# Performance work log

Measured on AMD Instinct MI355X. Metric: run time of the kernel, lower is better.

The kernel has to match this reference:

```python
import jax, jax.numpy as jnp
import numpy as np

B = 16          # number of point clouds in the batch
N_COARSE = 1024 # coarse points per cloud
N_FINE = 4096   # fine (skip) points per cloud
C_IN = 256
C_SKIP = 128
K = 3
EPS = 1e-16


def setup_inputs() -> dict:
    key = jax.random.key(0)
    ks = jax.random.split(key, 8)
    x = jax.random.normal(ks[0], (B * N_COARSE, C_IN), dtype=jnp.float32)
    pos = jax.random.uniform(ks[1], (B * N_COARSE, 3), dtype=jnp.float32)
    x_skip = jax.random.normal(ks[2], (B * N_FINE, C_SKIP), dtype=jnp.float32)
    pos_skip = jax.random.uniform(ks[3], (B * N_FINE, 3), dtype=jnp.float32)
    batch = jnp.repeat(jnp.arange(B, dtype=jnp.int64), N_COARSE)
    batch_skip = jnp.repeat(jnp.arange(B, dtype=jnp.int64), N_FINE)
    W1 = jax.random.normal(ks[4], (C_IN + C_SKIP, 256), dtype=jnp.float32) * (1.0 / np.sqrt(C_IN + C_SKIP))
    b1 = jnp.zeros((256,), dtype=jnp.float32)
    W2 = jax.random.normal(ks[5], (256, 256), dtype=jnp.float32) * (1.0 / np.sqrt(256))
    b2 = jnp.zeros((256,), dtype=jnp.float32)
    return {"x": x, "pos": pos, "batch": batch, "x_skip": x_skip,
            "pos_skip": pos_skip, "batch_skip": batch_skip,
            "W1": W1, "b1": b1, "W2": W2, "b2": b2}


def _knn_interpolate(x, pos, pos_skip):
    # Equal-sized clouds: reshape to [B, N, *] and do batched kNN.
    xc = x.reshape(B, N_COARSE, C_IN)
    pc = pos.reshape(B, N_COARSE, 3)
    pf = pos_skip.reshape(B, N_FINE, 3)
    # squared pairwise distances [B, M, N]
    d2 = (jnp.sum(pf * pf, -1)[:, :, None]
          + jnp.sum(pc * pc, -1)[:, None, :]
          - 2.0 * jnp.einsum('bmd,bnd->bmn', pf, pc))
    d2 = jnp.maximum(d2, 0.0)
    neg_d2k, idx = jax.lax.top_k(-d2, K)          # k smallest distances
    w = 1.0 / jnp.maximum(-neg_d2k, EPS)          # [B, M, K] inverse-sq-dist weights
    gathered = jax.vmap(lambda f, i: f[i])(xc, idx)  # [B, M, K, C]
    y = jnp.sum(w[..., None] * gathered, axis=2) / jnp.sum(w, axis=2, keepdims=True)
    return y.reshape(B * N_FINE, C_IN)


def reference(x, pos, batch, x_skip, pos_skip, batch_skip, W1, b1, W2, b2):
    x_interp = _knn_interpolate(x, pos, pos_skip)          # [B*M, C_IN]
    h = jnp.concatenate([x_interp, x_skip], axis=1)        # [B*M, C_IN + C_SKIP]
    h = jax.nn.relu(h @ W1 + b1)
    out = jax.nn.relu(h @ W2 + b2)
    return out
```

## Files before the change

### kernel.cpp

```cpp
#include <hip/hip_runtime.h>

typedef float  f32x4  __attribute__((ext_vector_type(4)));
typedef short  short8 __attribute__((ext_vector_type(8)));
typedef unsigned short ushort_t;
typedef ushort_t us4   __attribute__((ext_vector_type(4)));

#define NCOARSE 1024
#define NFINE   4096

__device__ __forceinline__ ushort_t f2bf(float f){
  union { float f; unsigned u; } a; a.f = f;
  unsigned u = a.u;
  return (ushort_t)((u + 0x7fffu + ((u >> 16) & 1u)) >> 16);
}

__device__ __forceinline__ f32x4 splat4(float v){ f32x4 t = {v, v, v, v}; return t; }

__global__ void prep_w2(const float* __restrict__ W1, const float* __restrict__ W2,
                        ushort_t* __restrict__ W1p, ushort_t* __restrict__ W2p){
  int e = blockIdx.x * 256 + threadIdx.x;
  const float* W; ushort_t* Wp; int idx;
  if (e < 98304){ W = W1; Wp = W1p; idx = e; }
  else          { W = W2; Wp = W2p; idx = e - 98304; }
  int j    = idx & 7;
  int lane = (idx >> 3) & 63;
  int g    = idx >> 9;
  int nb   = g & 15;
  int kc   = g >> 4;
  int k = kc * 32 + (lane >> 4) * 8 + j;
  int n = nb * 16 + (lane & 15);
  Wp[idx] = f2bf(W[k * 256 + n]);
}

#define LDW4(DST, WP, STEP)                                                   \
  { _Pragma("unroll")                                                         \
    for (int n_ = 0; n_ < 4; ++n_)                                            \
      DST[n_] = *(const short8*)((WP) +                                       \
          ((size_t)(((STEP) * 16 + wp * 4 + n_) * 64 + lane)) * 8); }

__global__ __launch_bounds__(256, 3)
void fp_fused(const float* __restrict__ pos, const float* __restrict__ pos_skip,
              const float* __restrict__ x, const float* __restrict__ x_skip,
              const ushort_t* __restrict__ W1p, const float* __restrict__ b1,
              const ushort_t* __restrict__ W2p, const float* __restrict__ b2,
              float* __restrict__ out){
  __shared__ __align__(16) ushort_t hbuf[32 * 384];
  char* h1b = (char*)hbuf;
  char* h2b = (char*)hbuf;
  f32x4* candp = (f32x4*)hbuf;
  const int tid  = threadIdx.x;
  const int lb   = ((blockIdx.x & 7) << 8) + (blockIdx.x >> 3);
  const int row0 = lb * 32;
  const int b    = lb >> 7;
  const int wp   = tid >> 6;
  const int lane = tid & 63;
  const int lhi  = lane >> 4;
  const int llo  = lane & 15;
  const int r    = tid >> 3;
  const int sub  = tid & 7;

  {
    const float* p = pos + (size_t)b * NCOARSE * 3;
    for (int c = tid; c < NCOARSE; c += 256){
      float xx = p[3*c], yy = p[3*c+1], zz = p[3*c+2];
      float sc = __fadd_rn(__fadd_rn(__fmul_rn(xx,xx), __fmul_rn(yy,yy)), __fmul_rn(zz,zz));
      f32x4 v = { xx, yy, zz, sc };
      candp[(c >> 7) * 129 + (c & 127)] = v;
    }
  }
  __syncthreads();

  float wn0, wn1, wn2;
  int   ig0, ig1, ig2;
  {
    const int m = row0 + r;
    const float* q = pos_skip + (size_t)m * 3;
    float qx = q[0], qy = q[1], qz = q[2];
    float sf = __fadd_rn(__fadd_rn(__fmul_rn(qx,qx), __fmul_rn(qy,qy)), __fmul_rn(qz,qz));

    float d0 = 1e30f, d1 = 1e30f, d2 = 1e30f;
    int   i0 = 0,     i1 = 0,     i2 = 0;
    const int gbase = sub * 128;
    #pragma unroll 4
    for (int i = 0; i < 128; ++i){
      f32x4 v = candp[sub * 129 + i];
      float dot = __fadd_rn(__fadd_rn(__fmul_rn(qx, v.x), __fmul_rn(qy, v.y)),
                            __fmul_rn(qz, v.z));
      float d = __fsub_rn(__fadd_rn(sf, v.w), __fmul_rn(2.0f, dot));
      d = fmaxf(d, 0.0f);
      if (d < d2){
        int gi = gbase + i;
        if (d < d1){
          d2 = d1; i2 = i1;
          if (d < d0){ d1 = d0; i1 = i0; d0 = d; i0 = gi; }
          else       { d1 = d;  i1 = gi; }
        } else { d2 = d; i2 = gi; }
      }
    }

    #pragma unroll
    for (int mlev = 1; mlev <= 4; mlev <<= 1){
      float e0 = __shfl_xor(d0, mlev), e1 = __shfl_xor(d1, mlev), e2 = __shfl_xor(d2, mlev);
      int   j0 = __shfl_xor(i0, mlev), j1 = __shfl_xor(i1, mlev), j2 = __shfl_xor(i2, mlev);
      #pragma unroll
      for (int s = 0; s < 3; ++s){
        float e = (s == 0) ? e0 : (s == 1) ? e1 : e2;
        int   j = (s == 0) ? j0 : (s == 1) ? j1 : j2;
        bool l2 = (e < d2) || (e == d2 && j < i2);
        if (l2){
          bool l1 = (e < d1) || (e == d1 && j < i1);
          if (l1){
            d2 = d1; i2 = i1;
            bool l0 = (e < d0) || (e == d0 && j < i0);
            if (l0){ d1 = d0; i1 = i0; d0 = e; i0 = j; }
            else   { d1 = e;  i1 = j; }
          } else { d2 = e; i2 = j; }
        }
      }
    }

    float w0 = 1.0f / fmaxf(d0, 1e-16f);
    float w1 = 1.0f / fmaxf(d1, 1e-16f);
    float w2 = 1.0f / fmaxf(d2, 1e-16f);
    float ws = __fadd_rn(__fadd_rn(w0, w1), w2);
    wn0 = w0 / ws; wn1 = w1 / ws; wn2 = w2 / ws;
    ig0 = b * NCOARSE + i0; ig1 = b * NCOARSE + i1; ig2 = b * NCOARSE + i2;
  }
  __syncthreads();

  {
    const int m = row0 + r;
    const f32x4* xsr = (const f32x4*)(x_skip + (size_t)m * 128);
    f32x4 xs[4];
    #pragma unroll
    for (int it = 0; it < 4; ++it) xs[it] = xsr[it * 8 + sub];
    const f32x4* x0 = (const f32x4*)(x + (size_t)ig0 * 256);
    const f32x4* x1 = (const f32x4*)(x + (size_t)ig1 * 256);
    const f32x4* x2 = (const f32x4*)(x + (size_t)ig2 * 256);
    #pragma unroll
    for (int it = 0; it < 8; ++it){
      int c4 = it * 8 + sub;
      f32x4 v = x0[c4] * wn0 + x1[c4] * wn1 + x2[c4] * wn2;
      int byte = (r * 768 + c4 * 8) ^ ((r & 7) << 4);
      us4 pk = { f2bf(v.x), f2bf(v.y), f2bf(v.z), f2bf(v.w) };
      *(us4*)(h1b + byte) = pk;
    }
    #pragma unroll
    for (int it = 0; it < 4; ++it){
      int c4 = it * 8 + sub;
      f32x4 v = xs[it];
      int byte = (r * 768 + 512 + c4 * 8) ^ ((r & 7) << 4);
      us4 pk = { f2bf(v.x), f2bf(v.y), f2bf(v.z), f2bf(v.w) };
      *(us4*)(h1b + byte) = pk;
    }
  }
  __syncthreads();

  f32x4 acc[2][4];
  #pragma unroll
  for (int nbp = 0; nbp < 4; ++nbp){
    float bb = b1[wp * 64 + nbp * 16 + llo];
    #pragma unroll
    for (int mb = 0; mb < 2; ++mb) acc[mb][nbp] = splat4(bb);
  }
  {
    short8 wr[3][4];
    LDW4(wr[0], W1p, 0);
    LDW4(wr[1], W1p, 1);
    LDW4(wr[2], W1p, 2);
    #pragma unroll
    for (int kk = 0; kk < 12; ++kk){
      short8 af[2];
      #pragma unroll
      for (int mb = 0; mb < 2; ++mb){
        int rr = mb * 16 + llo;
        int byte = (rr * 768 + kk * 64 + lhi * 16) ^ ((rr & 7) << 4);
        af[mb] = *(const short8*)(h1b + byte);
      }
      #pragma unroll
      for (int mb = 0; mb < 2; ++mb)
        #pragma unroll
        for (int nbp = 0; nbp < 4; ++nbp)
          acc[mb][nbp] = __builtin_amdgcn_mfma_f32_16x16x32_bf16(
              af[mb], wr[kk % 3][nbp], acc[mb][nbp], 0, 0, 0);
      if (kk + 3 < 12) { LDW4(wr[kk % 3], W1p, kk + 3); }
    }
  }
  __syncthreads();

  #pragma unroll
  for (int mb = 0; mb < 2; ++mb)
    #pragma unroll
    for (int nbp = 0; nbp < 4; ++nbp)
      #pragma unroll
      for (int rg = 0; rg < 4; ++rg){
        int rr  = mb * 16 + lhi * 4 + rg;
        int col = wp * 64 + nbp * 16 + llo;
        int byte = (rr * 512 + col * 2) ^ ((rr & 7) << 4);
        *(ushort_t*)(h2b + byte) = f2bf(fmaxf(acc[mb][nbp][rg], 0.0f));
      }
  __syncthreads();

  f32x4 acc2[2][4];
  #pragma unroll
  for (int nbp = 0; nbp < 4; ++nbp){
    float bb = b2[wp * 64 + nbp * 16 + llo];
    #pragma unroll
    for (int mb = 0; mb < 2; ++mb) acc2[mb][nbp] = splat4(bb);
  }
  {
    short8 wr[3][4];
    LDW4(wr[0], W2p, 0);
    LDW4(wr[1], W2p, 1);
    LDW4(wr[2], W2p, 2);
    #pragma unroll
    for (int kk = 0; kk < 8; ++kk){
      short8 af[2];
      #pragma unroll
      for (int mb = 0; mb < 2; ++mb){
        int rr = mb * 16 + llo;
        int byte = (rr * 512 + kk * 64 + lhi * 16) ^ ((rr & 7) << 4);
        af[mb] = *(const short8*)(h2b + byte);
      }
      #pragma unroll
      for (int mb = 0; mb < 2; ++mb)
        #pragma unroll
        for (int nbp = 0; nbp < 4; ++nbp)
          acc2[mb][nbp] = __builtin_amdgcn_mfma_f32_16x16x32_bf16(
              af[mb], wr[kk % 3][nbp], acc2[mb][nbp], 0, 0, 0);
      if (kk + 3 < 8) { LDW4(wr[kk % 3], W2p, kk + 3); }
    }
  }

  #pragma unroll
  for (int mb = 0; mb < 2; ++mb)
    #pragma unroll
    for (int nbp = 0; nbp < 4; ++nbp)
      #pragma unroll
      for (int rg = 0; rg < 4; ++rg){
        int row = row0 + mb * 16 + lhi * 4 + rg;
        int col = wp * 64 + nbp * 16 + llo;
        out[(size_t)row * 256 + col] = fmaxf(acc2[mb][nbp][rg], 0.0f);
      }
}

extern "C" void kernel_launch(void* const* d_in, const int* in_sizes, int n_in,
                              void* d_out, int out_size, void* d_ws, size_t ws_size,
                              hipStream_t stream){
  (void)in_sizes; (void)n_in; (void)out_size; (void)ws_size;
  const float* x        = (const float*)d_in[0];
  const float* pos      = (const float*)d_in[1];
  const float* x_skip   = (const float*)d_in[3];
  const float* pos_skip = (const float*)d_in[4];
  const float* W1 = (const float*)d_in[6];
  const float* b1 = (const float*)d_in[7];
  const float* W2 = (const float*)d_in[8];
  const float* b2 = (const float*)d_in[9];
  float* out = (float*)d_out;
  char* ws = (char*)d_ws;
  ushort_t* W1p = (ushort_t*)(ws);
  ushort_t* W2p = (ushort_t*)(ws + 196608);

  hipLaunchKernelGGL(prep_w2, dim3(640), dim3(256), 0, stream, W1, W2, W1p, W2p);
  hipLaunchKernelGGL(fp_fused, dim3(2048), dim3(256), 0, stream,
                     pos, pos_skip, x, x_skip, W1p, b1, W2p, b2, out);
}
```

Baseline: 78.83 us.

## Bucket coarse points by z and prune kNN scan to nearby slabs

Adds a prep kernel that sorts each cloud's coarse points into 32 z-slabs, using an atomic histogram and a prefix sum. The fused kernel then scans only the slabs near the query, and widens the search outward while a slab's z-gap could still beat the current third-best distance. This replaces the brute-force scan of all 1024 candidates per query. The x_skip load is also moved earlier so it overlaps the search. The cost is an extra launch, data-dependent loop lengths that can cause divergence, and a tie-break that now depends on lexicographic index comparison across buckets.

After: 81.87 us. 1.04x slower.

```diff
diff --git a/kernel.cpp b/kernel.cpp
--- a/kernel.cpp
+++ b/kernel.cpp
@@ -4,6 +4,7 @@
 typedef short  short8 __attribute__((ext_vector_type(8)));
 typedef unsigned short ushort_t;
 typedef ushort_t us4   __attribute__((ext_vector_type(4)));
+typedef int    int4v  __attribute__((ext_vector_type(4)));
 
 #define NCOARSE 1024
 #define NFINE   4096
@@ -32,14 +33,83 @@
   Wp[idx] = f2bf(W[k * 256 + n]);
 }
 
-#define LDW4(DST, WP, STEP)                                                   \
-  { _Pragma("unroll")                                                         \
-    for (int n_ = 0; n_ < 4; ++n_)                                            \
-      DST[n_] = *(const short8*)((WP) +                                       \
+__global__ __launch_bounds__(256) void prep_knn(const float* __restrict__ pos,
+                        f32x4* __restrict__ candS, int* __restrict__ idxS,
+                        int* __restrict__ offS){
+  __shared__ int hist[32], curs[32];
+  const int cl  = blockIdx.x;
+  const int tid = threadIdx.x;
+  const float* p = pos + (size_t)cl * NCOARSE * 3;
+  if (tid < 32) hist[tid] = 0;
+  __syncthreads();
+  for (int c = tid; c < NCOARSE; c += 256){
+    float z = p[3*c+2];
+    int bkt = min((int)(z * 32.0f), 31);
+    atomicAdd(&hist[bkt], 1);
+  }
+  __syncthreads();
+  if (tid == 0){
+    int acc = 0;
+    for (int bkt = 0; bkt < 32; ++bkt){
+      int h = hist[bkt]; hist[bkt] = acc; curs[bkt] = acc; acc += h;
+    }
+  }
+  __syncthreads();
+  if (tid < 32) offS[cl*33 + tid] = hist[tid];
+  if (tid == 0) offS[cl*33 + 32] = NCOARSE;
+  for (int c = tid; c < NCOARSE; c += 256){
+    float x = p[3*c], y = p[3*c+1], z = p[3*c+2];
+    float sc = __fadd_rn(__fadd_rn(__fmul_rn(x,x), __fmul_rn(y,y)), __fmul_rn(z,z));
+    int bkt = min((int)(z * 32.0f), 31);
+    int slot = atomicAdd(&curs[bkt], 1);
+    f32x4 v = { x, y, z, sc };
+    candS[(size_t)cl * NCOARSE + slot] = v;
+    idxS[(size_t)cl * NCOARSE + slot] = c;
+  }
+}
+
+#define LEXINS(D0,D1,D2,I0,I1,I2, E, J)                                     \
+  { bool l2_ = ((E) < D2) || ((E) == D2 && (J) < I2);                       \
+    if (l2_){                                                               \
+      bool l1_ = ((E) < D1) || ((E) == D1 && (J) < I1);                     \
+      if (l1_){                                                             \
+        D2 = D1; I2 = I1;                                                   \
+        bool l0_ = ((E) < D0) || ((E) == D0 && (J) < I0);                   \
+        if (l0_){ D1 = D0; I1 = I0; D0 = (E); I0 = (J); }                   \
+        else    { D1 = (E); I1 = (J); }                                     \
+      } else { D2 = (E); I2 = (J); }                                        \
+    } }
+
+#define BFLY_MERGE(D0,D1,D2,I0,I1,I2)                                       \
+  { _Pragma("unroll")                                                       \
+    for (int ml_ = 1; ml_ <= 4; ml_ <<= 1){                                 \
+      float m0_ = __shfl_xor(D0, ml_), m1_ = __shfl_xor(D1, ml_), m2_ = __shfl_xor(D2, ml_); \
+      int   n0_ = __shfl_xor(I0, ml_), n1_ = __shfl_xor(I1, ml_), n2_ = __shfl_xor(I2, ml_); \
+      LEXINS(D0,D1,D2,I0,I1,I2, m0_, n0_);                                  \
+      LEXINS(D0,D1,D2,I0,I1,I2, m1_, n1_);                                  \
+      LEXINS(D0,D1,D2,I0,I1,I2, m2_, n2_);                                  \
+    } }
+
+#define SCANB(BKT, D0,D1,D2,I0,I1,I2)                                       \
+  { int je_ = offL[(BKT)+1];                                                \
+    for (int j_ = offL[BKT] + sub; j_ < je_; j_ += 8){                      \
+      f32x4 v_ = candL[j_];                                                 \
+      float dt_ = __fadd_rn(__fadd_rn(__fmul_rn(qx, v_.x), __fmul_rn(qy, v_.y)), \
+                            __fmul_rn(qz, v_.z));                           \
+      float dd_ = fmaxf(__fsub_rn(__fadd_rn(sf, v_.w), __fmul_rn(2.0f, dt_)), 0.0f); \
+      int gi_ = idxL[j_];                                                   \
+      LEXINS(D0,D1,D2,I0,I1,I2, dd_, gi_);                                  \
+    } }
+
+#define LDW4(DST, WP, STEP)                                                 \
+  { _Pragma("unroll")                                                       \
+    for (int n_ = 0; n_ < 4; ++n_)                                          \
+      DST[n_] = *(const short8*)((WP) +                                     \
           ((size_t)(((STEP) * 16 + wp * 4 + n_) * 64 + lane)) * 8); }
 
 __global__ __launch_bounds__(256, 3)
-void fp_fused(const float* __restrict__ pos, const float* __restrict__ pos_skip,
+void fp_fused(const f32x4* __restrict__ candS, const int* __restrict__ idxS,
+              const int* __restrict__ offS, const float* __restrict__ pos_skip,
               const float* __restrict__ x, const float* __restrict__ x_skip,
               const ushort_t* __restrict__ W1p, const float* __restrict__ b1,
               const ushort_t* __restrict__ W2p, const float* __restrict__ b2,
@@ -47,7 +117,9 @@
   __shared__ __align__(16) ushort_t hbuf[32 * 384];
   char* h1b = (char*)hbuf;
   char* h2b = (char*)hbuf;
-  f32x4* candp = (f32x4*)hbuf;
+  f32x4* candL = (f32x4*)hbuf;
+  int*   idxL  = (int*)(h1b + 16384);
+  int*   offL  = (int*)(h1b + 20480);
   const int tid  = threadIdx.x;
   const int lb   = ((blockIdx.x & 7) << 8) + (blockIdx.x >> 3);
   const int row0 = lb * 32;
@@ -60,80 +132,68 @@
   const int sub  = tid & 7;
 
   {
-    const float* p = pos + (size_t)b * NCOARSE * 3;
-    for (int c = tid; c < NCOARSE; c += 256){
-      float xx = p[3*c], yy = p[3*c+1], zz = p[3*c+2];
-      float sc = __fadd_rn(__fadd_rn(__fmul_rn(xx,xx), __fmul_rn(yy,yy)), __fmul_rn(zz,zz));
-      f32x4 v = { xx, yy, zz, sc };
-      candp[(c >> 7) * 129 + (c & 127)] = v;
-    }
+    const f32x4* cs = candS + (size_t)b * NCOARSE;
+    const int4v* is = (const int4v*)(idxS + (size_t)b * NCOARSE);
+    #pragma unroll
+    for (int t = 0; t < 4; ++t) candL[t * 256 + tid] = cs[t * 256 + tid];
+    ((int4v*)idxL)[tid] = is[tid];
+    if (tid < 33) offL[tid] = offS[b * 33 + tid];
   }
   __syncthreads();
 
   float wn0, wn1, wn2;
   int   ig0, ig1, ig2;
+  f32x4 xs[4];
   {
     const int m = row0 + r;
+    const f32x4* xsr = (const f32x4*)(x_skip + (size_t)m * 128);
+    #pragma unroll
+    for (int it = 0; it < 4; ++it) xs[it] = xsr[it * 8 + sub];
+
     const float* q = pos_skip + (size_t)m * 3;
     float qx = q[0], qy = q[1], qz = q[2];
     float sf = __fadd_rn(__fadd_rn(__fmul_rn(qx,qx), __fmul_rn(qy,qy)), __fmul_rn(qz,qz));
 
     float d0 = 1e30f, d1 = 1e30f, d2 = 1e30f;
     int   i0 = 0,     i1 = 0,     i2 = 0;
-    const int gbase = sub * 128;
-    #pragma unroll 4
-    for (int i = 0; i < 128; ++i){
-      f32x4 v = candp[sub * 129 + i];
-      float dot = __fadd_rn(__fadd_rn(__fmul_rn(qx, v.x), __fmul_rn(qy, v.y)),
-                            __fmul_rn(qz, v.z));
-      float d = __fsub_rn(__fadd_rn(sf, v.w), __fmul_rn(2.0f, dot));
-      d = fmaxf(d, 0.0f);
-      if (d < d2){
-        int gi = gbase + i;
-        if (d < d1){
-          d2 = d1; i2 = i1;
-          if (d < d0){ d1 = d0; i1 = i0; d0 = d; i0 = gi; }
-          else       { d1 = d;  i1 = gi; }
-        } else { d2 = d; i2 = gi; }
-      }
-    }
-
-    #pragma unroll
-    for (int mlev = 1; mlev <= 4; mlev <<= 1){
-      float e0 = __shfl_xor(d0, mlev), e1 = __shfl_xor(d1, mlev), e2 = __shfl_xor(d2, mlev);
-      int   j0 = __shfl_xor(i0, mlev), j1 = __shfl_xor(i1, mlev), j2 = __shfl_xor(i2, mlev);
-      #pragma unroll
-      for (int s = 0; s < 3; ++s){
-        float e = (s == 0) ? e0 : (s == 1) ? e1 : e2;
-        int   j = (s == 0) ? j0 : (s == 1) ? j1 : j2;
-        bool l2 = (e < d2) || (e == d2 && j < i2);
-        if (l2){
-          bool l1 = (e < d1) || (e == d1 && j < i1);
-          if (l1){
-            d2 = d1; i2 = i1;
-            bool l0 = (e < d0) || (e == d0 && j < i0);
-            if (l0){ d1 = d0; i1 = i0; d0 = e; i0 = j; }
-            else   { d1 = e;  i1 = j; }
-          } else { d2 = e; i2 = j; }
-        }
-      }
-    }
-
-    float w0 = 1.0f / fmaxf(d0, 1e-16f);
-    float w1 = 1.0f / fmaxf(d1, 1e-16f);
-    float w2 = 1.0f / fmaxf(d2, 1e-16f);
+    int qb = min((int)(qz * 32.0f), 31);
+    int a0 = max(qb - 2, 0), a1 = min(qb + 2, 31);
+    for (int bkt = a0; bkt <= a1; ++bkt){ SCANB(bkt, d0,d1,d2,i0,i1,i2); }
+    BFLY_MERGE(d0,d1,d2,i0,i1,i2);
+
+    const float thr = __fadd_rn(d2, 1e-5f);
+    float e0 = 1e30f, e1 = 1e30f, e2 = 1e30f;
+    int   j0 = 0,     j1 = 0,     j2 = 0;
+    int bL = a0, bR = a1 + 1;
+    while (true){
+      bool canL = false, canR = false;
+      if (bL > 0){
+        float g = __fsub_rn(qz, (float)bL * 0.03125f);
+        canL = (__fmul_rn(g, g) < thr);
+      }
+      if (bR < 32){
+        float g = __fsub_rn((float)bR * 0.03125f, qz);
+        canR = (__fmul_rn(g, g) < thr);
+      }
+      if (!canL && !canR) break;
+      if (canL){ SCANB(bL - 1, e0,e1,e2,j0,j1,j2); --bL; }
+      if (canR){ SCANB(bR,     e0,e1,e2,j0,j1,j2); ++bR; }
+    }
+    BFLY_MERGE(e0,e1,e2,j0,j1,j2);
+    LEXINS(e0,e1,e2,j0,j1,j2, d0, i0);
+    LEXINS(e0,e1,e2,j0,j1,j2, d1, i1);
+    LEXINS(e0,e1,e2,j0,j1,j2, d2, i2);
+
+    float w0 = 1.0f / fmaxf(e0, 1e-16f);
+    float w1 = 1.0f / fmaxf(e1, 1e-16f);
+    float w2 = 1.0f / fmaxf(e2, 1e-16f);
     float ws = __fadd_rn(__fadd_rn(w0, w1), w2);
     wn0 = w0 / ws; wn1 = w1 / ws; wn2 = w2 / ws;
-    ig0 = b * NCOARSE + i0; ig1 = b * NCOARSE + i1; ig2 = b * NCOARSE + i2;
-  }
-  __syncthreads();
-
-  {
-    const int m = row0 + r;
-    const f32x4* xsr = (const f32x4*)(x_skip + (size_t)m * 128);
-    f32x4 xs[4];
-    #pragma unroll
-    for (int it = 0; it < 4; ++it) xs[it] = xsr[it * 8 + sub];
+    ig0 = b * NCOARSE + j0; ig1 = b * NCOARSE + j1; ig2 = b * NCOARSE + j2;
+  }
+  __syncthreads();
+
+  {
     const f32x4* x0 = (const f32x4*)(x + (size_t)ig0 * 256);
     const f32x4* x1 = (const f32x4*)(x + (size_t)ig1 * 256);
     const f32x4* x2 = (const f32x4*)(x + (size_t)ig2 * 256);
@@ -258,10 +318,14 @@
   const float* b2 = (const float*)d_in[9];
   float* out = (float*)d_out;
   char* ws = (char*)d_ws;
-  ushort_t* W1p = (ushort_t*)(ws);
-  ushort_t* W2p = (ushort_t*)(ws + 196608);
+  ushort_t* W1p  = (ushort_t*)(ws);
+  ushort_t* W2p  = (ushort_t*)(ws + 196608);
+  f32x4*    candS = (f32x4*)(ws + 327680);
+  int*      idxS  = (int*)(ws + 589824);
+  int*      offS  = (int*)(ws + 655360);
 
   hipLaunchKernelGGL(prep_w2, dim3(640), dim3(256), 0, stream, W1, W2, W1p, W2p);
+  hipLaunchKernelGGL(prep_knn, dim3(16), dim3(256), 0, stream, pos, candS, idxS, offS);
   hipLaunchKernelGGL(fp_fused, dim3(2048), dim3(256), 0, stream,
-                     pos, pos_skip, x, x_skip, W1p, b1, W2p, b2, out);
-}
+                     candS, idxS, offS, pos_skip, x, x_skip, W1p, b1, W2p, b2, out);
+}
```
